# Optimization experiments

Measured on AMD Instinct MI355X. Metric: run time of the kernel, lower is better.

## Reference

```python
import jax, jax.numpy as jnp
import numpy as np

N = 50000      # num_nodes
E = 400000     # num_edges
HDIM = 256     # h_dim
H = 4          # num_heads
D = HDIM // H  # per-head dim
NEG_SLOPE = 0.2  # DGL GATConv default leaky-relu slope


def setup_inputs() -> dict:
    key = jax.random.key(0)
    ks = jax.random.split(key, 12)
    sw = 1.0 / np.sqrt(HDIM)   # fan-in scaling for fc weights
    sa = 1.0 / np.sqrt(D)      # scaling for attention vectors
    return {
        "nids": jnp.arange(N, dtype=jnp.int32),
        "edge_src": jax.random.randint(ks[0], (E,), 0, N, dtype=jnp.int32),
        "edge_dst": jax.random.randint(ks[1], (E,), 0, N, dtype=jnp.int32),
        "emb": jax.random.normal(ks[2], (N, HDIM), jnp.float32),
        "W1": jax.random.normal(ks[3], (HDIM, HDIM), jnp.float32) * sw,
        "al1": jax.random.normal(ks[4], (H, D), jnp.float32) * sa,
        "ar1": jax.random.normal(ks[5], (H, D), jnp.float32) * sa,
        "b1": jnp.zeros((HDIM,), jnp.float32),
        "W2": jax.random.normal(ks[6], (HDIM, HDIM), jnp.float32) * sw,
        "al2": jax.random.normal(ks[7], (H, D), jnp.float32) * sa,
        "ar2": jax.random.normal(ks[8], (H, D), jnp.float32) * sa,
        "b2": jnp.zeros((HDIM,), jnp.float32),
    }


def _gat_layer(x, src, dst, W, al, ar, b):
    # DGL GATConv: fc -> per-head attn logits -> edge softmax over dst -> scatter-add
    f = (x @ W).reshape(-1, H, D)                       # [N,H,D]
    el = jnp.einsum('nhd,hd->nh', f, al)                # [N,H]
    er = jnp.einsum('nhd,hd->nh', f, ar)                # [N,H]
    e = jax.nn.leaky_relu(el[src] + er[dst], NEG_SLOPE) # [E,H]
    # segment softmax over incoming edges of each dst node
    m = jax.ops.segment_max(e, dst, num_segments=N)     # [N,H] (-inf for empty)
    ex = jnp.exp(e - m[dst])                            # [E,H]
    s = jax.ops.segment_sum(ex, dst, num_segments=N)    # [N,H]
    alpha = ex / s[dst]                                 # [E,H]
    msg = alpha[:, :, None] * f[src]                    # [E,H,D]
    out = jax.ops.segment_sum(msg, dst, num_segments=N) # [N,H,D]
    return out + b.reshape(1, H, D)


def reference(nids, edge_src, edge_dst, emb, W1, al1, ar1, b1, W2, al2, ar2, b2):
    x = emb[nids]                                        # embedding lookup [N,HDIM]
    h = _gat_layer(x, edge_src, edge_dst, W1, al1, ar1, b1)  # [N,H,D]
    h = jax.nn.elu(h)
    h = h.reshape(-1, HDIM)                              # concat heads for layer 2
    out = _gat_layer(h, edge_src, edge_dst, W2, al2, ar2, b2)  # [N,H,D]
    return out  # dropout is identity at inference
```

## Files before the change

### kernel.cpp

```cpp
#include <hip/hip_runtime.h>
#include <math.h>

#define NN 50000
#define EE 400000
#define HD 256
#define NH 4
#define DH 64
#define NEG_SLOPE 0.2f
#define NTILES 3125

typedef __attribute__((ext_vector_type(8))) _Float16 f16x8;
typedef __attribute__((ext_vector_type(4))) float f32x4;

__device__ __forceinline__ float bf2f(unsigned short h) {
  return __uint_as_float(((unsigned)h) << 16);
}
__device__ __forceinline__ unsigned short f2bf(float x) {
  __bf16 b = (__bf16)x;
  return *(unsigned short*)&b;
}

__global__ void k_zero_i32(int* __restrict__ p, int n) {
  int i = blockIdx.x * blockDim.x + threadIdx.x;
  if (i < n) p[i] = 0;
}

__global__ void k_count(const int* __restrict__ dst, int* __restrict__ counts,
                        int* __restrict__ rank) {
  int e = blockIdx.x * blockDim.x + threadIdx.x;
  if (e < EE) rank[e] = atomicAdd(&counts[dst[e]], 1);
}

__global__ void k_alloc(const int* __restrict__ counts, int* __restrict__ rstart,
                        int* __restrict__ total) {
  int i = blockIdx.x * blockDim.x + threadIdx.x;
  if (i < NN) rstart[i] = atomicAdd(total, counts[i]);
}

__global__ void k_scatter(const int* __restrict__ src, const int* __restrict__ dst,
                          const int* __restrict__ rstart, const int* __restrict__ rank,
                          int* __restrict__ csr_src) {
  int e = blockIdx.x * blockDim.x + threadIdx.x;
  if (e < EE) csr_src[rstart[dst[e]] + rank[e]] = src[e];
}

__global__ __launch_bounds__(256) void k_prep_w2(const float* __restrict__ W1,
                                                 const float* __restrict__ W2,
                                                 _Float16* __restrict__ W1t,
                                                 _Float16* __restrict__ W2t) {
  int b = blockIdx.x;
  const float* W = (b < 256) ? W1 : W2;
  _Float16* Wt = (b < 256) ? W1t : W2t;
  int t = (b & 255) * 256 + threadIdx.x;
  int n = t & 255, k = t >> 8;
  float x = W[(size_t)k * 256 + n];
  size_t o = (size_t)(k >> 5) * 8192 + (size_t)((k >> 3) & 3) * 2048 + (size_t)n * 8 + (k & 7);
  Wt[o] = (_Float16)x;
}

__device__ __forceinline__ void gload_lds16(const void* g, void* l) {
  __builtin_amdgcn_global_load_lds((const __attribute__((address_space(1))) void*)g,
                                   (__attribute__((address_space(3))) void*)l, 16, 0, 0);
}

template <int ABF16>
__global__ __launch_bounds__(768, 3) void k_gemm_mfma(
    const void* __restrict__ Av, const int* __restrict__ idx,
    const _Float16* __restrict__ Wt,
    const float* __restrict__ al, const float* __restrict__ ar,
    __bf16* __restrict__ C, float* __restrict__ el, float* __restrict__ er) {
  __shared__ f16x8 Bs[8192];

  int tid = threadIdx.x;
  int lane = tid & 63;
  int w = tid >> 6;
  int khalf = lane >> 4;
  int l15 = lane & 15;

  for (int i = tid; i < 8192; i += 768)
    gload_lds16(Wt + (size_t)i * 8, (void*)&Bs[i]);

  float alv[16], arv[16];
#pragma unroll
  for (int nf = 0; nf < 16; ++nf) {
    alv[nf] = al[nf * 16 + l15];
    arv[nf] = ar[nf * 16 + l15];
  }

  int nt = 1;
  int tiles[2];
  tiles[0] = blockIdx.x * 12 + w;
  int t2 = 3072 + blockIdx.x;
  if (w == 0 && t2 < NTILES) { tiles[1] = t2; nt = 2; }

  __syncthreads();

  for (int it = 0; it < nt; ++it) {
    int t = tiles[it];
    int row = t * 16 + l15;
    int arow = idx ? idx[row] : row;

    f32x4 acc[16];
#pragma unroll
    for (int nf = 0; nf < 16; ++nf) acc[nf] = (f32x4){0.f, 0.f, 0.f, 0.f};

    if (ABF16) {
      const __bf16* ap = (const __bf16*)Av + (size_t)arow * HD + khalf * 8;
#pragma unroll 2
      for (int kb = 0; kb < 8; ++kb) {
        ushort4 uv = *(const ushort4*)(ap + kb * 32);
        ushort4 uv2 = *(const ushort4*)(ap + kb * 32 + 4);
        f16x8 ah;
        ah[0] = (_Float16)bf2f(uv.x);
        ah[1] = (_Float16)bf2f(uv.y);
        ah[2] = (_Float16)bf2f(uv.z);
        ah[3] = (_Float16)bf2f(uv.w);
        ah[4] = (_Float16)bf2f(uv2.x);
        ah[5] = (_Float16)bf2f(uv2.y);
        ah[6] = (_Float16)bf2f(uv2.z);
        ah[7] = (_Float16)bf2f(uv2.w);
#pragma unroll
        for (int nf = 0; nf < 16; ++nf) {
          f16x8 bv = Bs[kb * 1024 + khalf * 256 + nf * 16 + l15];
          acc[nf] = __builtin_amdgcn_mfma_f32_16x16x32_f16(ah, bv, acc[nf], 0, 0, 0);
        }
      }
    } else {
      const float* ap = (const float*)Av + (size_t)arow * HD + khalf * 8;
#pragma unroll 2
      for (int kb = 0; kb < 8; ++kb) {
        float xx[8];
        *(float4*)&xx[0] = *(const float4*)(ap + kb * 32);
        *(float4*)&xx[4] = *(const float4*)(ap + kb * 32 + 4);
        f16x8 ah, alo;
#pragma unroll
        for (int i = 0; i < 8; ++i) {
          _Float16 h = (_Float16)xx[i];
          ah[i] = h;
          alo[i] = (_Float16)(xx[i] - (float)h);
        }
#pragma unroll
        for (int nf = 0; nf < 16; ++nf) {
          f16x8 bv = Bs[kb * 1024 + khalf * 256 + nf * 16 + l15];
          acc[nf] = __builtin_amdgcn_mfma_f32_16x16x32_f16(ah, bv, acc[nf], 0, 0, 0);
          acc[nf] = __builtin_amdgcn_mfma_f32_16x16x32_f16(alo, bv, acc[nf], 0, 0, 0);
        }
      }
    }

    int rowbase = t * 16 + khalf * 4;
#pragma unroll
    for (int r = 0; r < 4; ++r) {
      int row_ = rowbase + r;
      float seh[4], srh[4];
#pragma unroll
      for (int h = 0; h < 4; ++h) {
        float s1 = 0.f, s2 = 0.f;
#pragma unroll
        for (int j = 0; j < 4; ++j) {
          int nf = h * 4 + j;
          float v = acc[nf][r];
          s1 = fmaf(v, alv[nf], s1);
          s2 = fmaf(v, arv[nf], s2);
          C[(size_t)row_ * HD + nf * 16 + l15] = (__bf16)v;
        }
#pragma unroll
        for (int off = 1; off < 16; off <<= 1) {
          s1 += __shfl_xor(s1, off);
          s2 += __shfl_xor(s2, off);
        }
        seh[h] = s1;
        srh[h] = s2;
      }
      if (l15 == 0) {
        *(float4*)&el[row_ * NH] = make_float4(seh[0], seh[1], seh[2], seh[3]);
        *(float4*)&er[row_ * NH] = make_float4(srh[0], srh[1], srh[2], srh[3]);
      }
    }
  }
}

template <int OUTBF16>
__global__ __launch_bounds__(256) void k_aggregate(const __bf16* __restrict__ f,
                                                   const float* __restrict__ el,
                                                   const float* __restrict__ er,
                                                   const int* __restrict__ rstart,
                                                   const int* __restrict__ degs,
                                                   const int* __restrict__ csr_src,
                                                   const float* __restrict__ bias,
                                                   void* __restrict__ outv, int act) {
  int node = blockIdx.x * 4 + (threadIdx.x >> 6);
  if (node >= NN) return;
  int lane = threadIdx.x & 63;
  int start = rstart[node];
  int deg = degs[node];

  float ern = er[node * NH + (lane & 3)];

  int sreg[4];
  float ereg[4];
  float mloc = -INFINITY;
#pragma unroll
  for (int c = 0; c < 4; ++c) {
    int j = c * 16 + (lane >> 2);
    int s = 0;
    float e = -INFINITY;
    if (c * 16 < deg && j < deg) {
      s = csr_src[start + j];
      e = el[s * NH + (lane & 3)] + ern;
      e = (e >= 0.f) ? e : NEG_SLOPE * e;
    }
    sreg[c] = s;
    ereg[c] = e;
    mloc = fmaxf(mloc, e);
  }
  for (int j0 = 64; j0 < deg; j0 += 16) {
    int j = j0 + (lane >> 2);
    if (j < deg) {
      int s = csr_src[start + j];
      float e = el[s * NH + (lane & 3)] + ern;
      e = (e >= 0.f) ? e : NEG_SLOPE * e;
      mloc = fmaxf(mloc, e);
    }
  }
  float mm = mloc;
#pragma unroll
  for (int off = 4; off < 64; off <<= 1) mm = fmaxf(mm, __shfl_xor(mm, off));

  float vreg[4];
  float vloc = 0.f;
#pragma unroll
  for (int c = 0; c < 4; ++c) {
    float v = (ereg[c] > -INFINITY) ? __expf(ereg[c] - mm) : 0.f;
    vreg[c] = v;
    vloc += v;
  }
  for (int j0 = 64; j0 < deg; j0 += 16) {
    int j = j0 + (lane >> 2);
    if (j < deg) {
      int s = csr_src[start + j];
      float e = el[s * NH + (lane & 3)] + ern;
      e = (e >= 0.f) ? e : NEG_SLOPE * e;
      vloc += __expf(e - mm);
    }
  }
  float ss = vloc;
#pragma unroll
  for (int off = 4; off < 64; off <<= 1) ss += __shfl_xor(ss, off);

  float inv_own = (ss > 0.f) ? (1.f / ss) : 0.f;
  float areg[4];
#pragma unroll
  for (int c = 0; c < 4; ++c) areg[c] = vreg[c] * inv_own;

  int head = lane >> 4;

  float4 acc = ((const float4*)bias)[lane];
  for (int c = 0; c < 4; ++c) {
    int base = c * 16;
    if (base >= deg) break;
    int cnt = deg - base;
    cnt = (cnt > 16) ? 16 : cnt;
    for (int g = 0; g < cnt; g += 8) {
      ushort4 u[8];
      float aa[8];
#pragma unroll
      for (int jj = 0; jj < 8; ++jj) {
        int j = g + jj;
        int jc = (j < cnt) ? j : (cnt - 1);
        int srcl = jc * 4 + head;
        int s = __shfl(sreg[c], srcl);
        float a = __shfl(areg[c], srcl);
        aa[jj] = (j < cnt) ? a : 0.f;
        u[jj] = ((const ushort4*)(f + (size_t)s * HD))[lane];
      }
#pragma unroll
      for (int jj = 0; jj < 8; ++jj) {
        acc.x = fmaf(aa[jj], bf2f(u[jj].x), acc.x);
        acc.y = fmaf(aa[jj], bf2f(u[jj].y), acc.y);
        acc.z = fmaf(aa[jj], bf2f(u[jj].z), acc.z);
        acc.w = fmaf(aa[jj], bf2f(u[jj].w), acc.w);
      }
    }
  }
  if (deg > 64) {
    float mH = __shfl(mm, head);
    float sH = __shfl(ss, head);
    float erH = __shfl(ern, head);
    float invH = (sH > 0.f) ? (1.f / sH) : 0.f;
    for (int j = 64; j < deg; ++j) {
      int s = csr_src[start + j];
      float e = el[s * NH + head] + erH;
      e = (e >= 0.f) ? e : NEG_SLOPE * e;
      float a = __expf(e - mH) * invH;
      ushort4 u = ((const ushort4*)(f + (size_t)s * HD))[lane];
      acc.x = fmaf(a, bf2f(u.x), acc.x);
      acc.y = fmaf(a, bf2f(u.y), acc.y);
      acc.z = fmaf(a, bf2f(u.z), acc.z);
      acc.w = fmaf(a, bf2f(u.w), acc.w);
    }
  }

  if (act) {
    acc.x = (acc.x > 0.f) ? acc.x : __expf(acc.x) - 1.f;
    acc.y = (acc.y > 0.f) ? acc.y : __expf(acc.y) - 1.f;
    acc.z = (acc.z > 0.f) ? acc.z : __expf(acc.z) - 1.f;
    acc.w = (acc.w > 0.f) ? acc.w : __expf(acc.w) - 1.f;
  }
  if (OUTBF16) {
    ushort4 st;
    st.x = f2bf(acc.x);
    st.y = f2bf(acc.y);
    st.z = f2bf(acc.z);
    st.w = f2bf(acc.w);
    ((ushort4*)((__bf16*)outv + (size_t)node * HD))[lane] = st;
  } else {
    ((float4*)((float*)outv + (size_t)node * HD))[lane] = acc;
  }
}

extern "C" void kernel_launch(void* const* d_in, const int* in_sizes, int n_in,
                              void* d_out, int out_size, void* d_ws, size_t ws_size,
                              hipStream_t stream) {
  const int* nids = (const int*)d_in[0];
  const int* esrc = (const int*)d_in[1];
  const int* edst = (const int*)d_in[2];
  const float* emb = (const float*)d_in[3];
  const float* W1 = (const float*)d_in[4];
  const float* al1 = (const float*)d_in[5];
  const float* ar1 = (const float*)d_in[6];
  const float* b1 = (const float*)d_in[7];
  const float* W2 = (const float*)d_in[8];
  const float* al2 = (const float*)d_in[9];
  const float* ar2 = (const float*)d_in[10];
  const float* b2 = (const float*)d_in[11];
  float* out = (float*)d_out;

  char* w = (char*)d_ws;
  size_t off = 0;
  auto alloc = [&](size_t bytes) {
    void* p = w + off;
    off += (bytes + 255) & ~(size_t)255;
    return p;
  };
  __bf16* fbuf = (__bf16*)alloc((size_t)NN * HD * 2);
  __bf16* hbuf = (__bf16*)alloc((size_t)NN * HD * 2);
  float* el = (float*)alloc((size_t)NN * NH * 4);
  float* er = (float*)alloc((size_t)NN * NH * 4);
  int* rstart = (int*)alloc((size_t)NN * 4);
  int* counts = (int*)alloc((size_t)(NN + 8) * 4);
  int* total = counts + NN;
  int* rank = (int*)alloc((size_t)EE * 4);
  int* csr_src = (int*)alloc((size_t)EE * 4);
  _Float16* W1t = (_Float16*)alloc((size_t)HD * HD * 2);
  _Float16* W2t = (_Float16*)alloc((size_t)HD * HD * 2);

  int nbE = (EE + 255) / 256;

  k_zero_i32<<<(NN + 8 + 255) / 256, 256, 0, stream>>>(counts, NN + 8);
  k_count<<<nbE, 256, 0, stream>>>(edst, counts, rank);
  k_alloc<<<(NN + 255) / 256, 256, 0, stream>>>(counts, rstart, total);
  k_scatter<<<nbE, 256, 0, stream>>>(esrc, edst, rstart, rank, csr_src);
  k_prep_w2<<<512, 256, 0, stream>>>(W1, W2, W1t, W2t);

  int nbNode4 = (NN + 3) / 4;

  k_gemm_mfma<0><<<256, 768, 0, stream>>>(emb, nids, W1t, al1, ar1, fbuf, el, er);
  k_aggregate<1><<<nbNode4, 256, 0, stream>>>(fbuf, el, er, rstart, counts, csr_src, b1, hbuf, 1);

  k_gemm_mfma<1><<<256, 768, 0, stream>>>(hbuf, nullptr, W2t, al2, ar2, fbuf, el, er);
  k_aggregate<0><<<nbNode4, 256, 0, stream>>>(fbuf, el, er, rstart, counts, csr_src, b2, out, 0);
}
```

Before: 180.3 us.

## Merge init kernels, widen GEMM blocks to 1024 threads, prefetch A rows

Fuses the count-zeroing and weight-transpose kernels into one launch, which saves a kernel launch. The MFMA GEMM now runs 1024-thread blocks (16 waves, one tile each) over 196 blocks. This replaces the uneven 12-wave layout in which one wave per block picked up a second tail tile. The A-row loads are software-prefetched one k-step ahead with full unrolling, and bf16 unpacking uses 32-bit shifts/masks. The changes aim to cut launch overhead, tail imbalance and load latency, at the cost of higher register pressure under the 1024-thread launch bound.

```diff
diff --git a/kernel.cpp b/kernel.cpp
--- a/kernel.cpp
+++ b/kernel.cpp
@@ -20,9 +20,25 @@
   return *(unsigned short*)&b;
 }
 
-__global__ void k_zero_i32(int* __restrict__ p, int n) {
-  int i = blockIdx.x * blockDim.x + threadIdx.x;
-  if (i < n) p[i] = 0;
+__global__ __launch_bounds__(256) void k_init(int* __restrict__ counts,
+                                              const float* __restrict__ W1,
+                                              const float* __restrict__ W2,
+                                              _Float16* __restrict__ W1t,
+                                              _Float16* __restrict__ W2t) {
+  int b = blockIdx.x;
+  if (b < 196) {
+    int i = b * 256 + threadIdx.x;
+    if (i < NN + 8) counts[i] = 0;
+  } else {
+    int bb = b - 196;
+    const float* W = (bb < 256) ? W1 : W2;
+    _Float16* Wt = (bb < 256) ? W1t : W2t;
+    int t = (bb & 255) * 256 + threadIdx.x;
+    int n = t & 255, k = t >> 8;
+    float x = W[(size_t)k * 256 + n];
+    size_t o = (size_t)(k >> 5) * 8192 + (size_t)((k >> 3) & 3) * 2048 + (size_t)n * 8 + (k & 7);
+    Wt[o] = (_Float16)x;
+  }
 }
 
 __global__ void k_count(const int* __restrict__ dst, int* __restrict__ counts,
@@ -44,27 +60,13 @@
   if (e < EE) csr_src[rstart[dst[e]] + rank[e]] = src[e];
 }
 
-__global__ __launch_bounds__(256) void k_prep_w2(const float* __restrict__ W1,
-                                                 const float* __restrict__ W2,
-                                                 _Float16* __restrict__ W1t,
-                                                 _Float16* __restrict__ W2t) {
-  int b = blockIdx.x;
-  const float* W = (b < 256) ? W1 : W2;
-  _Float16* Wt = (b < 256) ? W1t : W2t;
-  int t = (b & 255) * 256 + threadIdx.x;
-  int n = t & 255, k = t >> 8;
-  float x = W[(size_t)k * 256 + n];
-  size_t o = (size_t)(k >> 5) * 8192 + (size_t)((k >> 3) & 3) * 2048 + (size_t)n * 8 + (k & 7);
-  Wt[o] = (_Float16)x;
-}
-
 __device__ __forceinline__ void gload_lds16(const void* g, void* l) {
   __builtin_amdgcn_global_load_lds((const __attribute__((address_space(1))) void*)g,
                                    (__attribute__((address_space(3))) void*)l, 16, 0, 0);
 }
 
 template <int ABF16>
-__global__ __launch_bounds__(768, 3) void k_gemm_mfma(
+__global__ __launch_bounds__(1024, 4) void k_gemm_mfma(
     const void* __restrict__ Av, const int* __restrict__ idx,
     const _Float16* __restrict__ Wt,
     const float* __restrict__ al, const float* __restrict__ ar,
@@ -77,7 +79,7 @@
   int khalf = lane >> 4;
   int l15 = lane & 15;
 
-  for (int i = tid; i < 8192; i += 768)
+  for (int i = tid; i < 8192; i += 1024)
     gload_lds16(Wt + (size_t)i * 8, (void*)&Bs[i]);
 
   float alv[16], arv[16];
@@ -87,16 +89,12 @@
     arv[nf] = ar[nf * 16 + l15];
   }
 
-  int nt = 1;
-  int tiles[2];
-  tiles[0] = blockIdx.x * 12 + w;
-  int t2 = 3072 + blockIdx.x;
-  if (w == 0 && t2 < NTILES) { tiles[1] = t2; nt = 2; }
+  int t = blockIdx.x * 16 + w;
+  bool active = t < NTILES;
 
   __syncthreads();
 
-  for (int it = 0; it < nt; ++it) {
-    int t = tiles[it];
+  if (active) {
     int row = t * 16 + l15;
     int arow = idx ? idx[row] : row;
 
@@ -106,32 +104,39 @@
 
     if (ABF16) {
       const __bf16* ap = (const __bf16*)Av + (size_t)arow * HD + khalf * 8;
-#pragma unroll 2
+      uint4 cur = *(const uint4*)(ap);
+#pragma unroll
       for (int kb = 0; kb < 8; ++kb) {
-        ushort4 uv = *(const ushort4*)(ap + kb * 32);
-        ushort4 uv2 = *(const ushort4*)(ap + kb * 32 + 4);
+        uint4 nxt;
+        if (kb < 7) nxt = *(const uint4*)(ap + (kb + 1) * 32);
+        const unsigned* uu = (const unsigned*)&cur;
         f16x8 ah;
-        ah[0] = (_Float16)bf2f(uv.x);
-        ah[1] = (_Float16)bf2f(uv.y);
-        ah[2] = (_Float16)bf2f(uv.z);
-        ah[3] = (_Float16)bf2f(uv.w);
-        ah[4] = (_Float16)bf2f(uv2.x);
-        ah[5] = (_Float16)bf2f(uv2.y);
-        ah[6] = (_Float16)bf2f(uv2.z);
-        ah[7] = (_Float16)bf2f(uv2.w);
+#pragma unroll
+        for (int i = 0; i < 4; ++i) {
+          ah[2 * i] = (_Float16)__uint_as_float(uu[i] << 16);
+          ah[2 * i + 1] = (_Float16)__uint_as_float(uu[i] & 0xffff0000u);
+        }
 #pragma unroll
         for (int nf = 0; nf < 16; ++nf) {
           f16x8 bv = Bs[kb * 1024 + khalf * 256 + nf * 16 + l15];
           acc[nf] = __builtin_amdgcn_mfma_f32_16x16x32_f16(ah, bv, acc[nf], 0, 0, 0);
         }
+        cur = nxt;
       }
     } else {
       const float* ap = (const float*)Av + (size_t)arow * HD + khalf * 8;
-#pragma unroll 2
+      float4 c0 = *(const float4*)(ap);
+      float4 c1 = *(const float4*)(ap + 4);
+#pragma unroll
       for (int kb = 0; kb < 8; ++kb) {
+        float4 n0, n1;
+        if (kb < 7) {
+          n0 = *(const float4*)(ap + (kb + 1) * 32);
+          n1 = *(const float4*)(ap + (kb + 1) * 32 + 4);
+        }
         float xx[8];
-        *(float4*)&xx[0] = *(const float4*)(ap + kb * 32);
-        *(float4*)&xx[4] = *(const float4*)(ap + kb * 32 + 4);
+        *(float4*)&xx[0] = c0;
+        *(float4*)&xx[4] = c1;
         f16x8 ah, alo;
 #pragma unroll
         for (int i = 0; i < 8; ++i) {
@@ -145,6 +150,8 @@
           acc[nf] = __builtin_amdgcn_mfma_f32_16x16x32_f16(ah, bv, acc[nf], 0, 0, 0);
           acc[nf] = __builtin_amdgcn_mfma_f32_16x16x32_f16(alo, bv, acc[nf], 0, 0, 0);
         }
+        c0 = n0;
+        c1 = n1;
       }
     }
 
@@ -357,17 +364,16 @@
 
   int nbE = (EE + 255) / 256;
 
-  k_zero_i32<<<(NN + 8 + 255) / 256, 256, 0, stream>>>(counts, NN + 8);
+  k_init<<<708, 256, 0, stream>>>(counts, W1, W2, W1t, W2t);
   k_count<<<nbE, 256, 0, stream>>>(edst, counts, rank);
   k_alloc<<<(NN + 255) / 256, 256, 0, stream>>>(counts, rstart, total);
   k_scatter<<<nbE, 256, 0, stream>>>(esrc, edst, rstart, rank, csr_src);
-  k_prep_w2<<<512, 256, 0, stream>>>(W1, W2, W1t, W2t);
 
   int nbNode4 = (NN + 3) / 4;
 
-  k_gemm_mfma<0><<<256, 768, 0, stream>>>(emb, nids, W1t, al1, ar1, fbuf, el, er);
+  k_gemm_mfma<0><<<196, 1024, 0, stream>>>(emb, nids, W1t, al1, ar1, fbuf, el, er);
   k_aggregate<1><<<nbNode4, 256, 0, stream>>>(fbuf, el, er, rstart, counts, csr_src, b1, hbuf, 1);
 
-  k_gemm_mfma<1><<<256, 768, 0, stream>>>(hbuf, nullptr, W2t, al2, ar2, fbuf, el, er);
+  k_gemm_mfma<1><<<196, 1024, 0, stream>>>(hbuf, nullptr, W2t, al2, ar2, fbuf, el, er);
   k_aggregate<0><<<nbNode4, 256, 0, stream>>>(fbuf, el, er, rstart, counts, csr_src, b2, out, 0);
 }
```

Measured after the change: 173.5 us. 1.04x faster.
